# Performance work log

Measured on AMD Instinct MI355X. Metric: run time of the kernel, lower is better.

Reference implementation:

```python
import jax, jax.numpy as jnp
import numpy as np

N_NODES = 100000
N_EDGES = 800000


def gcn_conv(x, W, b, src, dst, ew, n):
    # PyG GCNConv with edge weights and self-loops already included in (src, dst, ew):
    # deg[i] = sum of incoming edge weights at i; norm_e = d^-1/2[src] * w_e * d^-1/2[dst]
    h = x @ W                                                  # [N, F_out]
    deg = jax.ops.segment_sum(ew, dst, num_segments=n)         # [N]
    dinv = jnp.where(deg > 0, jax.lax.rsqrt(deg), 0.0)
    norm = dinv[src] * ew * dinv[dst]                          # [E]
    out = jax.ops.segment_sum(h[src] * norm[:, None], dst, num_segments=n)
    return out + b


def add_self_loops(edge_index, edge_weight, n):
    loop = jnp.arange(n, dtype=edge_index.dtype)
    src = jnp.concatenate([edge_index[0], loop])
    dst = jnp.concatenate([edge_index[1], loop])
    ew = jnp.concatenate([edge_weight, jnp.ones((n,), edge_weight.dtype)])
    return src, dst, ew


def setup_inputs() -> dict:
    key = jax.random.key(0)
    ks = jax.random.split(key, 10)
    x = jax.random.normal(ks[0], (N_NODES, 5), jnp.float32)
    edge_index = jax.random.randint(ks[1], (2, N_EDGES), 0, N_NODES, dtype=jnp.int64)
    edge_weight = jax.random.uniform(ks[2], (N_EDGES,), jnp.float32)
    def glorot(k, fan_in, fan_out):
        s = float(np.sqrt(6.0 / (fan_in + fan_out)))
        return jax.random.uniform(k, (fan_in, fan_out), jnp.float32, -s, s)
    return {
        "x": x,
        "edge_index": edge_index,
        "edge_weight": edge_weight,
        "W1": glorot(ks[3], 5, 320),
        "b1": jnp.zeros((320,), jnp.float32),
        "W2": glorot(ks[4], 320, 160),
        "b2": jnp.zeros((160,), jnp.float32),
        "We": glorot(ks[5], 160, 80),
        "be": jnp.zeros((80,), jnp.float32),
    }


def reference(x, edge_index, edge_weight, W1, b1, W2, b2, We, be):
    n = x.shape[0]
    src, dst, ew = add_self_loops(edge_index, edge_weight, n)
    h = gcn_conv(x, W1, b1, src, dst, ew, n)        # conv1
    h = jax.nn.relu(h)
    h = gcn_conv(h, W2, b2, src, dst, ew, n)        # conv2
    return h @ We + be                              # embed linear
```

## Files before the change

### kernel.cpp

```cpp
#include <hip/hip_runtime.h>

#define NF0 5
#define F1 320
#define F2 160
#define F3 80

typedef float f32x4 __attribute__((ext_vector_type(4)));
typedef _Float16 f16x8 __attribute__((ext_vector_type(8)));


__global__ void k_binA(const void* ei, const float* __restrict__ ew, const int* __restrict__ flag,
                       int* __restrict__ bin_cnt , int2* __restrict__ bins,
                       int bin_stride, int* __restrict__ ovf_n, int* __restrict__ ovf,
                       int ovf_cap, int E) {
    int e = blockIdx.x * blockDim.x + threadIdx.x;
    if (e >= E) return;
    int s, d;
    if (*flag) {
        const long long* p = (const long long*)ei;
        s = (int)p[e]; d = (int)p[E + e];
    } else {
        const int* p = (const int*)ei;
        s = p[e]; d = p[E + e];
    }
    float w = ew[e];
    int b = d >> 8;
    int pos = atomicAdd(&bin_cnt[b * 16], 1);
    if (pos < bin_stride) {
        int2 pk;
        pk.x = s | ((d & 255) << 24);
        pk.y = __float_as_int(w);
        bins[(size_t)b * bin_stride + pos] = pk;
    } else {
        int o = atomicAdd(ovf_n, 1);
        if (o < ovf_cap) {
            ovf[3 * o] = s; ovf[3 * o + 1] = d; ovf[3 * o + 2] = __float_as_int(w);
        }
    }
}

__global__ void k_fixdeg(const int* __restrict__ ovf_n, const int* __restrict__ ovf, int ovf_cap,
                         float* __restrict__ deg) {
    int n = *ovf_n; if (n > ovf_cap) n = ovf_cap;
    for (int j = blockIdx.x * blockDim.x + threadIdx.x; j < n; j += gridDim.x * blockDim.x)
        atomicAdd(&deg[ovf[3 * j + 1]], __int_as_float(ovf[3 * j + 2]));
}


__global__ __launch_bounds__(256) void k_binB1(const int2* __restrict__ bins, int bin_stride,
                                               const int* __restrict__ bin_cnt,
                                               float* __restrict__ deg ,
                                               int N) {
    __shared__ float deg_l[256];
    int b = blockIdx.x, t = threadIdx.x;
    deg_l[t] = 0.f;
    __syncthreads();
    int ne = bin_cnt[b * 16]; if (ne > bin_stride) ne = bin_stride;
    const int2* bp = bins + (size_t)b * bin_stride;
    for (int j = t; j < ne; j += 256) {
        int2 pk = bp[j];
        atomicAdd(&deg_l[((unsigned int)pk.x) >> 24], __int_as_float(pk.y));
    }
    __syncthreads();
    int node = b * 256 + t;
    if (node < N) deg[node] = rsqrtf(deg[node] + 1.0f + deg_l[t]);
}


__global__ __launch_bounds__(256) void k_binB2(const int2* __restrict__ bins, int bin_stride,
                                               const int* __restrict__ bin_cnt,
                                               const float* __restrict__ dinv,
                                               const float* __restrict__ xp,
                                               int* __restrict__ cnt, int2* __restrict__ bucket,
                                               int cap, float* __restrict__ agg1,
                                               int* __restrict__ ovf_n, int* __restrict__ ovf,
                                               int ovf_cap, int N) {
    __shared__ int cnt_l[256];
    __shared__ float dinv_l[256];
    __shared__ float acc_l[256 * NF0];
    int b = blockIdx.x, t = threadIdx.x;
    cnt_l[t] = 0;
    int node0 = b * 256 + t;
    dinv_l[t] = (node0 < N) ? dinv[node0] : 0.f;
    for (int q = t; q < 256 * NF0; q += 256) acc_l[q] = 0.f;
    __syncthreads();

    int ne = bin_cnt[b * 16]; if (ne > bin_stride) ne = bin_stride;
    const int2* bp = bins + (size_t)b * bin_stride;
    for (int j = t; j < ne; j += 256) {
        int2 pk = bp[j];
        int s = pk.x & 0xFFFFFF;
        int dl = ((unsigned int)pk.x) >> 24;
        float w = dinv[s] * __int_as_float(pk.y) * dinv_l[dl];
        int node = b * 256 + dl;
        int pos = atomicAdd(&cnt_l[dl], 1);
        if (pos < cap) {
            int2 out_pk; out_pk.x = s; out_pk.y = __float_as_int(w);
            bucket[(size_t)node * cap + pos] = out_pk;
        } else {
            int o = atomicAdd(ovf_n, 1);
            if (o < ovf_cap) { ovf[3 * o] = s; ovf[3 * o + 1] = node; ovf[3 * o + 2] = pk.y; }
        }
        float4 sv = *(const float4*)(xp + (size_t)s * 8);
        float s4 = xp[(size_t)s * 8 + 4];
        atomicAdd(&acc_l[dl * NF0 + 0], sv.x * w);
        atomicAdd(&acc_l[dl * NF0 + 1], sv.y * w);
        atomicAdd(&acc_l[dl * NF0 + 2], sv.z * w);
        atomicAdd(&acc_l[dl * NF0 + 3], sv.w * w);
        atomicAdd(&acc_l[dl * NF0 + 4], s4 * w);
    }
    __syncthreads();

    if (node0 < N) {
        float di = dinv_l[t];
        float sc = di * di;
        float4 xv = *(const float4*)(xp + (size_t)node0 * 8);
        float x4 = xp[(size_t)node0 * 8 + 4];
        float* op = agg1 + (size_t)node0 * NF0;
        op[0] = acc_l[t * NF0 + 0] + xv.x * sc;
        op[1] = acc_l[t * NF0 + 1] + xv.y * sc;
        op[2] = acc_l[t * NF0 + 2] + xv.z * sc;
        op[3] = acc_l[t * NF0 + 3] + xv.w * sc;
        op[4] = acc_l[t * NF0 + 4] + x4 * sc;
        int c = cnt_l[t]; if (c > cap) c = cap;
        cnt[node0] = c;
    }
}


__global__ void k_prep(const float* __restrict__ x, float* __restrict__ xp, int N, int padxB,
                       const float* __restrict__ W2, const float* __restrict__ We,
                       _Float16* __restrict__ Bh,
                       const float* __restrict__ b2, const float* __restrict__ be,
                       float* __restrict__ bc,
                       const unsigned int* __restrict__ ei32, int E, int* __restrict__ flag) {
    __shared__ int ok;
    int b = blockIdx.x;
    if (b < padxB) {
        int t = b * 256 + threadIdx.x;
        if (t < N * 8) {
            int f = t & 7, i = t >> 3;
            xp[t] = (f < NF0) ? x[i * NF0 + f] : 0.f;
        }
    } else if (b < padxB + 13) {
        int t = (b - padxB) * 256 + threadIdx.x;
        if (t >= 50 * 64) return;
        int fid = t >> 6, lane = t & 63;
        int kk = fid / 5, ct = fid % 5;
        int col = ct * 16 + (lane & 15);
        int row0 = kk * 32 + (lane >> 4) * 8;
        float acc[8] = {0.f, 0.f, 0.f, 0.f, 0.f, 0.f, 0.f, 0.f};
        for (int m = 0; m < F2; ++m) {
            float wv = We[m * F3 + col];
            #pragma unroll
            for (int i = 0; i < 8; ++i)
                acc[i] += W2[(size_t)(row0 + i) * F2 + m] * wv;
        }
        size_t ob = (size_t)t * 8;
        #pragma unroll
        for (int i = 0; i < 8; ++i)
            Bh[ob + i] = (_Float16)acc[i];
    } else if (b == padxB + 13) {
        int j = threadIdx.x;
        if (j < F3) {
            float s = be[j];
            for (int k = 0; k < F2; ++k) s += b2[k] * We[k * F3 + j];
            bc[j] = s;
        }
    } else {
        if (threadIdx.x == 0) ok = 1;
        __syncthreads();
        int npairs = E < 2048 ? E : 2048;
        for (int i = threadIdx.x; i < npairs; i += blockDim.x)
            if (ei32[2 * i + 1] != 0u) ok = 0;
        __syncthreads();
        if (threadIdx.x == 0) *flag = ok;
    }
}

__global__ void k_fixA(const float* __restrict__ x, const float* __restrict__ dinv,
                       const int* __restrict__ ovf_n, int* __restrict__ ovf, int ovf_cap,
                       float* __restrict__ agg1) {
    int n = *ovf_n; if (n > ovf_cap) n = ovf_cap;
    for (int j = blockIdx.x * blockDim.x + threadIdx.x; j < n; j += gridDim.x * blockDim.x) {
        int s = ovf[3 * j], d = ovf[3 * j + 1];
        float w = dinv[s] * __int_as_float(ovf[3 * j + 2]) * dinv[d];
        ovf[3 * j + 2] = __float_as_int(w);
        #pragma unroll
        for (int f = 0; f < NF0; ++f)
            atomicAdd(&agg1[(size_t)d * NF0 + f], x[(size_t)s * NF0 + f] * w);
    }
}


__global__ __launch_bounds__(256) void k_node(const float* __restrict__ agg1,
                                              const float* __restrict__ W1,
                                              const float* __restrict__ b1,
                                              const _Float16* __restrict__ Bh,
                                              _Float16* __restrict__ g, int N) {
    __shared__ float W_l[6 * F1];
    int tid = threadIdx.x;
    for (int i = tid; i < 480; i += 256) {
        float4 v = (i < 400) ? ((const float4*)W1)[i] : ((const float4*)b1)[i - 400];
        ((float4*)W_l)[i] = v;
    }
    __syncthreads();

    int w = tid >> 6, l = tid & 63;
    int nl = l & 15, kg = l >> 4;
    int base = blockIdx.x * 64 + w * 16;
    int n0 = base + nl;

    float a0v[5] = {0.f, 0.f, 0.f, 0.f, 0.f};
    if (n0 < N) {
        const float* ap = agg1 + (size_t)n0 * NF0;
        #pragma unroll
        for (int j = 0; j < 5; ++j) a0v[j] = ap[j];
    }

    f32x4 zero = {0.f, 0.f, 0.f, 0.f};
    f32x4 acc[5] = {zero, zero, zero, zero, zero};
    const f16x8* bhp = (const f16x8*)Bh;

    #pragma unroll
    for (int kk = 0; kk < 10; ++kk) {
        int k0 = kk * 32 + kg * 8;
        float v0[8];
        const float* bb = W_l + 5 * F1 + k0;
        #pragma unroll
        for (int i = 0; i < 8; ++i) v0[i] = bb[i];
        #pragma unroll
        for (int j = 0; j < 5; ++j) {
            const float* wp = W_l + j * F1 + k0;
            float aj0 = a0v[j];
            #pragma unroll
            for (int i = 0; i < 8; ++i) v0[i] += aj0 * wp[i];
        }
        f16x8 ah0, al0;
        #pragma unroll
        for (int i = 0; i < 8; ++i) {
            float t0 = fmaxf(v0[i], 0.f);
            _Float16 h0 = (_Float16)t0;
            ah0[i] = h0;
            al0[i] = (_Float16)(t0 - (float)h0);
        }
        #pragma unroll
        for (int ct = 0; ct < 5; ++ct) {
            f16x8 bf = bhp[(kk * 5 + ct) * 64 + l];
            acc[ct] = __builtin_amdgcn_mfma_f32_16x16x32_f16(ah0, bf, acc[ct], 0, 0, 0);
            acc[ct] = __builtin_amdgcn_mfma_f32_16x16x32_f16(al0, bf, acc[ct], 0, 0, 0);
        }
    }

    #pragma unroll
    for (int ct = 0; ct < 5; ++ct) {
        #pragma unroll
        for (int r = 0; r < 4; ++r) {
            int r0 = base + kg * 4 + r;
            if (r0 < N) g[(size_t)r0 * F3 + ct * 16 + nl] = (_Float16)acc[ct][r];
        }
    }
}


__global__ __launch_bounds__(256) void k_aggB(const _Float16* __restrict__ g,
                                              const float* __restrict__ dinv,
                                              const float* __restrict__ bc,
                                              const int* __restrict__ cnt,
                                              const int2* __restrict__ bucket, int cap,
                                              float* __restrict__ out, int N) {
    int t = blockIdx.x * blockDim.x + threadIdx.x;
    if (t >= 5 * N) return;
    int i = t / 5;
    int c = (t - i * 5) << 4;
    float di = dinv[i];
    float sc = di * di;
    float acc[16];
    {
        const f16x8* sp = (const f16x8*)(g + (size_t)i * F3 + c);
        f16x8 u0 = sp[0], u1 = sp[1];
        const float4* bp = (const float4*)(bc + c);
        float4 q0 = bp[0], q1 = bp[1], q2 = bp[2], q3 = bp[3];
        acc[0]  = (float)u0[0] * sc + q0.x;  acc[1]  = (float)u0[1] * sc + q0.y;
        acc[2]  = (float)u0[2] * sc + q0.z;  acc[3]  = (float)u0[3] * sc + q0.w;
        acc[4]  = (float)u0[4] * sc + q1.x;  acc[5]  = (float)u0[5] * sc + q1.y;
        acc[6]  = (float)u0[6] * sc + q1.z;  acc[7]  = (float)u0[7] * sc + q1.w;
        acc[8]  = (float)u1[0] * sc + q2.x;  acc[9]  = (float)u1[1] * sc + q2.y;
        acc[10] = (float)u1[2] * sc + q2.z;  acc[11] = (float)u1[3] * sc + q2.w;
        acc[12] = (float)u1[4] * sc + q3.x;  acc[13] = (float)u1[5] * sc + q3.y;
        acc[14] = (float)u1[6] * sc + q3.z;  acc[15] = (float)u1[7] * sc + q3.w;
    }
    int cn = cnt[i];
    const int2* row = bucket + (size_t)i * cap;
    #pragma unroll 2
    for (int j = 0; j < cn; ++j) {
        int2 pk = row[j];
        float w = __int_as_float(pk.y);
        const f16x8* sp = (const f16x8*)(g + (size_t)pk.x * F3 + c);
        f16x8 a = sp[0], b8 = sp[1];
        #pragma unroll
        for (int e = 0; e < 8; ++e) {
            acc[e]     += (float)a[e]  * w;
            acc[8 + e] += (float)b8[e] * w;
        }
    }
    float4* op = (float4*)(out + (size_t)i * F3 + c);
    #pragma unroll
    for (int q = 0; q < 4; ++q) {
        float4 v;
        v.x = acc[q * 4 + 0]; v.y = acc[q * 4 + 1]; v.z = acc[q * 4 + 2]; v.w = acc[q * 4 + 3];
        op[q] = v;
    }
}

__global__ void k_fixB(const _Float16* __restrict__ g, const float* __restrict__ dinv,
                       const int* __restrict__ ovf_n, const int* __restrict__ ovf, int ovf_cap,
                       float* __restrict__ out) {
    int n = *ovf_n; if (n > ovf_cap) n = ovf_cap;
    for (int j = blockIdx.x * blockDim.x + threadIdx.x; j < n; j += gridDim.x * blockDim.x) {
        int s = ovf[3 * j], d = ovf[3 * j + 1];
        float w = __int_as_float(ovf[3 * j + 2]);
        for (int f = 0; f < F3; ++f)
            atomicAdd(&out[(size_t)d * F3 + f], (float)g[(size_t)s * F3 + f] * w);
    }
}


static inline size_t align256(size_t x) { return (x + 255) & ~(size_t)255; }

extern "C" void kernel_launch(void* const* d_in, const int* in_sizes, int n_in,
                              void* d_out, int out_size, void* d_ws, size_t ws_size,
                              hipStream_t stream) {
    const float* x  = (const float*)d_in[0];
    const void*  ei = d_in[1];
    const float* ew = (const float*)d_in[2];
    const float* W1 = (const float*)d_in[3];
    const float* b1 = (const float*)d_in[4];
    const float* W2 = (const float*)d_in[5];
    const float* b2 = (const float*)d_in[6];
    const float* We = (const float*)d_in[7];
    const float* be = (const float*)d_in[8];
    float* out = (float*)d_out;

    int N = in_sizes[0] / NF0;
    int E = in_sizes[2];

    const int OVF_CAP = 131072;
    const int BIN_STRIDE = 4096;
    int n_bins = (N + 255) >> 8;

    char* p = (char*)d_ws;
    auto alloc = [&](size_t bytes) { char* r = p; p += align256(bytes); return r; };
    int*   flag  = (int*)alloc(4);
    size_t zints = (size_t)N + 16 + (size_t)n_bins * 16;
    int*   zreg  = (int*)alloc(zints * 4);
    float* deg   = (float*)zreg;
    int*   ovf_n = zreg + N;
    int*   bin_cnt = zreg + N + 16;
    int*   cnt   = (int*)  alloc((size_t)N * 4);
    int*   ovf   = (int*)  alloc((size_t)OVF_CAP * 12);
    int2*  bins  = (int2*) alloc((size_t)n_bins * BIN_STRIDE * 8);
    float* xp    = (float*)alloc((size_t)N * 8 * 4);
    float* agg1  = (float*)alloc((size_t)N * NF0 * 4);
    float* bc    = (float*)alloc((size_t)F3 * 4);
    _Float16* Bh = (_Float16*)alloc((size_t)50 * 64 * 8 * 2);
    _Float16* g  = (_Float16*)alloc((size_t)N * F3 * 2);

    size_t used = (size_t)(p - (char*)d_ws);
    int cap = 24;
    if (ws_size > used) {
        size_t avail = (ws_size - used) / ((size_t)N * 8);
        if (avail < (size_t)cap) cap = (int)avail;
    } else cap = 4;
    if (cap < 4) cap = 4;
    int2* bucket = (int2*)alloc((size_t)N * cap * 8);

    int eb  = (E + 255) / 256;
    int padxB = (N * 8 + 255) / 256;

    hipMemsetAsync(zreg, 0, zints * 4, stream);
    k_prep<<<padxB + 15, 256, 0, stream>>>(x, xp, N, padxB, W2, We, Bh, b2, be, bc,
                                           (const unsigned int*)ei, E, flag);

    k_binA<<<eb, 256, 0, stream>>>(ei, ew, flag, bin_cnt, bins, BIN_STRIDE, ovf_n, ovf, OVF_CAP, E);
    k_fixdeg<<<16, 256, 0, stream>>>(ovf_n, ovf, OVF_CAP, deg);
    k_binB1<<<n_bins, 256, 0, stream>>>(bins, BIN_STRIDE, bin_cnt, deg, N);
    k_binB2<<<n_bins, 256, 0, stream>>>(bins, BIN_STRIDE, bin_cnt, deg, xp, cnt, bucket, cap,
                                        agg1, ovf_n, ovf, OVF_CAP, N);
    k_fixA<<<16, 256, 0, stream>>>(x, deg, ovf_n, ovf, OVF_CAP, agg1);

    k_node<<<(N + 63) / 64, 256, 0, stream>>>(agg1, W1, b1, Bh, g, N);
    k_aggB<<<(5 * N + 255) / 256, 256, 0, stream>>>(g, deg, bc, cnt, bucket, cap, out, N);
    k_fixB<<<16, 256, 0, stream>>>(g, deg, ovf_n, ovf, OVF_CAP, out);
}
```

Baseline: 189.3 us.

## Factor symmetric normalization into node scaling and split edge bins into sub-bins

The symmetric normalization is factored so that source features are pre-scaled by dinv (xp in binB1, g in k_node) and the destination dinv is applied once per node. Edge weights therefore no longer need per-edge dinv gathers. Edge bins are split into 8 sub-bins chosen by block index, to spread the atomic counter contention in binA. The memset and the separate fixdeg and fixA kernels are folded into prep, binB1 and binB2, which now scan the overflow list per block. This cuts launches and global atomics, but every bin block rescans the whole overflow list, and the smaller per-sub-bin capacity may send more edges to overflow.

```diff
diff --git a/kernel.cpp b/kernel.cpp
--- a/kernel.cpp
+++ b/kernel.cpp
@@ -4,131 +4,15 @@
 #define F1 320
 #define F2 160
 #define F3 80
+#define NSUB 8
+#define SUBCAP 512
 
 typedef float f32x4 __attribute__((ext_vector_type(4)));
 typedef _Float16 f16x8 __attribute__((ext_vector_type(8)));
 
 
-__global__ void k_binA(const void* ei, const float* __restrict__ ew, const int* __restrict__ flag,
-                       int* __restrict__ bin_cnt , int2* __restrict__ bins,
-                       int bin_stride, int* __restrict__ ovf_n, int* __restrict__ ovf,
-                       int ovf_cap, int E) {
-    int e = blockIdx.x * blockDim.x + threadIdx.x;
-    if (e >= E) return;
-    int s, d;
-    if (*flag) {
-        const long long* p = (const long long*)ei;
-        s = (int)p[e]; d = (int)p[E + e];
-    } else {
-        const int* p = (const int*)ei;
-        s = p[e]; d = p[E + e];
-    }
-    float w = ew[e];
-    int b = d >> 8;
-    int pos = atomicAdd(&bin_cnt[b * 16], 1);
-    if (pos < bin_stride) {
-        int2 pk;
-        pk.x = s | ((d & 255) << 24);
-        pk.y = __float_as_int(w);
-        bins[(size_t)b * bin_stride + pos] = pk;
-    } else {
-        int o = atomicAdd(ovf_n, 1);
-        if (o < ovf_cap) {
-            ovf[3 * o] = s; ovf[3 * o + 1] = d; ovf[3 * o + 2] = __float_as_int(w);
-        }
-    }
-}
-
-__global__ void k_fixdeg(const int* __restrict__ ovf_n, const int* __restrict__ ovf, int ovf_cap,
-                         float* __restrict__ deg) {
-    int n = *ovf_n; if (n > ovf_cap) n = ovf_cap;
-    for (int j = blockIdx.x * blockDim.x + threadIdx.x; j < n; j += gridDim.x * blockDim.x)
-        atomicAdd(&deg[ovf[3 * j + 1]], __int_as_float(ovf[3 * j + 2]));
-}
-
-
-__global__ __launch_bounds__(256) void k_binB1(const int2* __restrict__ bins, int bin_stride,
-                                               const int* __restrict__ bin_cnt,
-                                               float* __restrict__ deg ,
-                                               int N) {
-    __shared__ float deg_l[256];
-    int b = blockIdx.x, t = threadIdx.x;
-    deg_l[t] = 0.f;
-    __syncthreads();
-    int ne = bin_cnt[b * 16]; if (ne > bin_stride) ne = bin_stride;
-    const int2* bp = bins + (size_t)b * bin_stride;
-    for (int j = t; j < ne; j += 256) {
-        int2 pk = bp[j];
-        atomicAdd(&deg_l[((unsigned int)pk.x) >> 24], __int_as_float(pk.y));
-    }
-    __syncthreads();
-    int node = b * 256 + t;
-    if (node < N) deg[node] = rsqrtf(deg[node] + 1.0f + deg_l[t]);
-}
-
-
-__global__ __launch_bounds__(256) void k_binB2(const int2* __restrict__ bins, int bin_stride,
-                                               const int* __restrict__ bin_cnt,
-                                               const float* __restrict__ dinv,
-                                               const float* __restrict__ xp,
-                                               int* __restrict__ cnt, int2* __restrict__ bucket,
-                                               int cap, float* __restrict__ agg1,
-                                               int* __restrict__ ovf_n, int* __restrict__ ovf,
-                                               int ovf_cap, int N) {
-    __shared__ int cnt_l[256];
-    __shared__ float dinv_l[256];
-    __shared__ float acc_l[256 * NF0];
-    int b = blockIdx.x, t = threadIdx.x;
-    cnt_l[t] = 0;
-    int node0 = b * 256 + t;
-    dinv_l[t] = (node0 < N) ? dinv[node0] : 0.f;
-    for (int q = t; q < 256 * NF0; q += 256) acc_l[q] = 0.f;
-    __syncthreads();
-
-    int ne = bin_cnt[b * 16]; if (ne > bin_stride) ne = bin_stride;
-    const int2* bp = bins + (size_t)b * bin_stride;
-    for (int j = t; j < ne; j += 256) {
-        int2 pk = bp[j];
-        int s = pk.x & 0xFFFFFF;
-        int dl = ((unsigned int)pk.x) >> 24;
-        float w = dinv[s] * __int_as_float(pk.y) * dinv_l[dl];
-        int node = b * 256 + dl;
-        int pos = atomicAdd(&cnt_l[dl], 1);
-        if (pos < cap) {
-            int2 out_pk; out_pk.x = s; out_pk.y = __float_as_int(w);
-            bucket[(size_t)node * cap + pos] = out_pk;
-        } else {
-            int o = atomicAdd(ovf_n, 1);
-            if (o < ovf_cap) { ovf[3 * o] = s; ovf[3 * o + 1] = node; ovf[3 * o + 2] = pk.y; }
-        }
-        float4 sv = *(const float4*)(xp + (size_t)s * 8);
-        float s4 = xp[(size_t)s * 8 + 4];
-        atomicAdd(&acc_l[dl * NF0 + 0], sv.x * w);
-        atomicAdd(&acc_l[dl * NF0 + 1], sv.y * w);
-        atomicAdd(&acc_l[dl * NF0 + 2], sv.z * w);
-        atomicAdd(&acc_l[dl * NF0 + 3], sv.w * w);
-        atomicAdd(&acc_l[dl * NF0 + 4], s4 * w);
-    }
-    __syncthreads();
-
-    if (node0 < N) {
-        float di = dinv_l[t];
-        float sc = di * di;
-        float4 xv = *(const float4*)(xp + (size_t)node0 * 8);
-        float x4 = xp[(size_t)node0 * 8 + 4];
-        float* op = agg1 + (size_t)node0 * NF0;
-        op[0] = acc_l[t * NF0 + 0] + xv.x * sc;
-        op[1] = acc_l[t * NF0 + 1] + xv.y * sc;
-        op[2] = acc_l[t * NF0 + 2] + xv.z * sc;
-        op[3] = acc_l[t * NF0 + 3] + xv.w * sc;
-        op[4] = acc_l[t * NF0 + 4] + x4 * sc;
-        int c = cnt_l[t]; if (c > cap) c = cap;
-        cnt[node0] = c;
-    }
-}
-
-
-__global__ void k_prep(const float* __restrict__ x, float* __restrict__ xp, int N, int padxB,
+__global__ void k_prep(const float* __restrict__ x, float* __restrict__ xp, int N,
+                       int padz, int* __restrict__ zreg, int zwords, int padxB,
                        const float* __restrict__ W2, const float* __restrict__ We,
                        _Float16* __restrict__ Bh,
                        const float* __restrict__ b2, const float* __restrict__ be,
@@ -136,6 +20,12 @@
                        const unsigned int* __restrict__ ei32, int E, int* __restrict__ flag) {
     __shared__ int ok;
     int b = blockIdx.x;
+    if (b < padz) {
+        int t = b * 256 + threadIdx.x;
+        if (t < zwords) zreg[t] = 0;
+        return;
+    }
+    b -= padz;
     if (b < padxB) {
         int t = b * 256 + threadIdx.x;
         if (t < N * 8) {
@@ -178,17 +68,151 @@
     }
 }
 
-__global__ void k_fixA(const float* __restrict__ x, const float* __restrict__ dinv,
-                       const int* __restrict__ ovf_n, int* __restrict__ ovf, int ovf_cap,
-                       float* __restrict__ agg1) {
+
+__global__ void k_binA(const void* ei, const float* __restrict__ ew, const int* __restrict__ flag,
+                       int* __restrict__ bin_cnt , int2* __restrict__ bins,
+                       int n_bins, int* __restrict__ ovf_n, int* __restrict__ ovf,
+                       int ovf_cap, int E) {
+    int e = blockIdx.x * blockDim.x + threadIdx.x;
+    if (e >= E) return;
+    int sub = blockIdx.x & (NSUB - 1);
+    int s, d;
+    if (*flag) {
+        const long long* p = (const long long*)ei;
+        s = (int)p[e]; d = (int)p[E + e];
+    } else {
+        const int* p = (const int*)ei;
+        s = p[e]; d = p[E + e];
+    }
+    float w = ew[e];
+    int b = d >> 8;
+    int pos = atomicAdd(&bin_cnt[(sub * n_bins + b) * 4], 1);
+    if (pos < SUBCAP) {
+        int2 pk;
+        pk.x = s | ((d & 255) << 24);
+        pk.y = __float_as_int(w);
+        bins[(size_t)b * (NSUB * SUBCAP) + sub * SUBCAP + pos] = pk;
+    } else {
+        int o = atomicAdd(ovf_n, 1);
+        if (o < ovf_cap) {
+            ovf[3 * o] = s; ovf[3 * o + 1] = d; ovf[3 * o + 2] = __float_as_int(w);
+        }
+    }
+}
+
+
+__global__ __launch_bounds__(256) void k_binB1(const int2* __restrict__ bins,
+                                               const int* __restrict__ bin_cnt, int n_bins,
+                                               float* __restrict__ dinv, float* __restrict__ xp,
+                                               const int* __restrict__ ovf_n,
+                                               const int* __restrict__ ovf, int ovf_cap, int N) {
+    __shared__ float deg_l[256];
+    int b = blockIdx.x, t = threadIdx.x;
+    deg_l[t] = 0.f;
+    __syncthreads();
+    for (int sub = 0; sub < NSUB; ++sub) {
+        int ne = bin_cnt[(sub * n_bins + b) * 4]; if (ne > SUBCAP) ne = SUBCAP;
+        const int2* bp = bins + (size_t)b * (NSUB * SUBCAP) + sub * SUBCAP;
+        for (int j = t; j < ne; j += 256) {
+            int2 pk = bp[j];
+            atomicAdd(&deg_l[((unsigned int)pk.x) >> 24], __int_as_float(pk.y));
+        }
+    }
     int n = *ovf_n; if (n > ovf_cap) n = ovf_cap;
-    for (int j = blockIdx.x * blockDim.x + threadIdx.x; j < n; j += gridDim.x * blockDim.x) {
-        int s = ovf[3 * j], d = ovf[3 * j + 1];
-        float w = dinv[s] * __int_as_float(ovf[3 * j + 2]) * dinv[d];
-        ovf[3 * j + 2] = __float_as_int(w);
-        #pragma unroll
-        for (int f = 0; f < NF0; ++f)
-            atomicAdd(&agg1[(size_t)d * NF0 + f], x[(size_t)s * NF0 + f] * w);
+    int lo = b * 256;
+    for (int j = t; j < n; j += 256) {
+        int d = ovf[3 * j + 1];
+        if (d >= lo && d < lo + 256)
+            atomicAdd(&deg_l[d - lo], __int_as_float(ovf[3 * j + 2]));
+    }
+    __syncthreads();
+    int node = lo + t;
+    if (node < N) {
+        float di = rsqrtf(1.0f + deg_l[t]);
+        dinv[node] = di;
+        float4* xr = (float4*)(xp + (size_t)node * 8);
+        float4 v0 = xr[0], v1 = xr[1];
+        v0.x *= di; v0.y *= di; v0.z *= di; v0.w *= di;
+        v1.x *= di; v1.y *= di; v1.z *= di; v1.w *= di;
+        xr[0] = v0; xr[1] = v1;
+    }
+}
+
+
+__global__ __launch_bounds__(256) void k_binB2(const int2* __restrict__ bins,
+                                               const int* __restrict__ bin_cnt, int n_bins,
+                                               const float* __restrict__ dinv,
+                                               const float* __restrict__ xp,
+                                               int* __restrict__ cnt, int2* __restrict__ bucket,
+                                               int cap, float* __restrict__ agg1,
+                                               int* __restrict__ ovf_n, int* __restrict__ ovf,
+                                               int ovf_cap, int N) {
+    __shared__ int cnt_l[256];
+    __shared__ float acc_l[256 * NF0];
+    int b = blockIdx.x, t = threadIdx.x;
+    cnt_l[t] = 0;
+    for (int q = t; q < 256 * NF0; q += 256) acc_l[q] = 0.f;
+    int nsnap = *ovf_n; if (nsnap > ovf_cap) nsnap = ovf_cap;
+    __syncthreads();
+    int lo = b * 256;
+
+    for (int j = t; j < nsnap; j += 256) {
+        int d = ovf[3 * j + 1];
+        if (d >= lo && d < lo + 256) {
+            int s = ovf[3 * j];
+            float w = __int_as_float(ovf[3 * j + 2]);
+            float4 sv = *(const float4*)(xp + (size_t)s * 8);
+            float s4 = xp[(size_t)s * 8 + 4];
+            int dl = d - lo;
+            atomicAdd(&acc_l[dl * NF0 + 0], sv.x * w);
+            atomicAdd(&acc_l[dl * NF0 + 1], sv.y * w);
+            atomicAdd(&acc_l[dl * NF0 + 2], sv.z * w);
+            atomicAdd(&acc_l[dl * NF0 + 3], sv.w * w);
+            atomicAdd(&acc_l[dl * NF0 + 4], s4 * w);
+        }
+    }
+
+    for (int sub = 0; sub < NSUB; ++sub) {
+        int ne = bin_cnt[(sub * n_bins + b) * 4]; if (ne > SUBCAP) ne = SUBCAP;
+        const int2* bp = bins + (size_t)b * (NSUB * SUBCAP) + sub * SUBCAP;
+        for (int j = t; j < ne; j += 256) {
+            int2 pk = bp[j];
+            int s = pk.x & 0xFFFFFF;
+            int dl = ((unsigned int)pk.x) >> 24;
+            float w = __int_as_float(pk.y);
+            int node = lo + dl;
+            int pos = atomicAdd(&cnt_l[dl], 1);
+            if (pos < cap) {
+                int2 out_pk; out_pk.x = s; out_pk.y = pk.y;
+                bucket[(size_t)node * cap + pos] = out_pk;
+            } else {
+                int o = atomicAdd(ovf_n, 1);
+                if (o < ovf_cap) { ovf[3 * o] = s; ovf[3 * o + 1] = node; ovf[3 * o + 2] = pk.y; }
+            }
+            float4 sv = *(const float4*)(xp + (size_t)s * 8);
+            float s4 = xp[(size_t)s * 8 + 4];
+            atomicAdd(&acc_l[dl * NF0 + 0], sv.x * w);
+            atomicAdd(&acc_l[dl * NF0 + 1], sv.y * w);
+            atomicAdd(&acc_l[dl * NF0 + 2], sv.z * w);
+            atomicAdd(&acc_l[dl * NF0 + 3], sv.w * w);
+            atomicAdd(&acc_l[dl * NF0 + 4], s4 * w);
+        }
+    }
+    __syncthreads();
+
+    int node = lo + t;
+    if (node < N) {
+        float di = dinv[node];
+        float4 xv = *(const float4*)(xp + (size_t)node * 8);
+        float x4 = xp[(size_t)node * 8 + 4];
+        float* op = agg1 + (size_t)node * NF0;
+        op[0] = di * (acc_l[t * NF0 + 0] + xv.x);
+        op[1] = di * (acc_l[t * NF0 + 1] + xv.y);
+        op[2] = di * (acc_l[t * NF0 + 2] + xv.z);
+        op[3] = di * (acc_l[t * NF0 + 3] + xv.w);
+        op[4] = di * (acc_l[t * NF0 + 4] + x4);
+        int c = cnt_l[t]; if (c > cap) c = cap;
+        cnt[node] = c;
     }
 }
 
@@ -197,6 +221,7 @@
                                               const float* __restrict__ W1,
                                               const float* __restrict__ b1,
                                               const _Float16* __restrict__ Bh,
+                                              const float* __restrict__ dinv,
                                               _Float16* __restrict__ g, int N) {
     __shared__ float W_l[6 * F1];
     int tid = threadIdx.x;
@@ -253,11 +278,13 @@
     }
 
     #pragma unroll
-    for (int ct = 0; ct < 5; ++ct) {
-        #pragma unroll
-        for (int r = 0; r < 4; ++r) {
-            int r0 = base + kg * 4 + r;
-            if (r0 < N) g[(size_t)r0 * F3 + ct * 16 + nl] = (_Float16)acc[ct][r];
+    for (int r = 0; r < 4; ++r) {
+        int r0 = base + kg * 4 + r;
+        if (r0 < N) {
+            float dv = dinv[r0];
+            #pragma unroll
+            for (int ct = 0; ct < 5; ++ct)
+                g[(size_t)r0 * F3 + ct * 16 + nl] = (_Float16)(acc[ct][r] * dv);
         }
     }
 }
@@ -273,23 +300,9 @@
     if (t >= 5 * N) return;
     int i = t / 5;
     int c = (t - i * 5) << 4;
-    float di = dinv[i];
-    float sc = di * di;
     float acc[16];
-    {
-        const f16x8* sp = (const f16x8*)(g + (size_t)i * F3 + c);
-        f16x8 u0 = sp[0], u1 = sp[1];
-        const float4* bp = (const float4*)(bc + c);
-        float4 q0 = bp[0], q1 = bp[1], q2 = bp[2], q3 = bp[3];
-        acc[0]  = (float)u0[0] * sc + q0.x;  acc[1]  = (float)u0[1] * sc + q0.y;
-        acc[2]  = (float)u0[2] * sc + q0.z;  acc[3]  = (float)u0[3] * sc + q0.w;
-        acc[4]  = (float)u0[4] * sc + q1.x;  acc[5]  = (float)u0[5] * sc + q1.y;
-        acc[6]  = (float)u0[6] * sc + q1.z;  acc[7]  = (float)u0[7] * sc + q1.w;
-        acc[8]  = (float)u1[0] * sc + q2.x;  acc[9]  = (float)u1[1] * sc + q2.y;
-        acc[10] = (float)u1[2] * sc + q2.z;  acc[11] = (float)u1[3] * sc + q2.w;
-        acc[12] = (float)u1[4] * sc + q3.x;  acc[13] = (float)u1[5] * sc + q3.y;
-        acc[14] = (float)u1[6] * sc + q3.z;  acc[15] = (float)u1[7] * sc + q3.w;
-    }
+    #pragma unroll
+    for (int e = 0; e < 16; ++e) acc[e] = 0.f;
     int cn = cnt[i];
     const int2* row = bucket + (size_t)i * cap;
     #pragma unroll 2
@@ -304,13 +317,30 @@
             acc[8 + e] += (float)b8[e] * w;
         }
     }
+    float di = dinv[i];
+    const f16x8* sp = (const f16x8*)(g + (size_t)i * F3 + c);
+    f16x8 u0 = sp[0], u1 = sp[1];
+    const float4* bp = (const float4*)(bc + c);
+    float4 q0 = bp[0], q1 = bp[1], q2 = bp[2], q3 = bp[3];
+    float4 o0, o1, o2, o3;
+    o0.x = di * (acc[0]  + (float)u0[0]) + q0.x;
+    o0.y = di * (acc[1]  + (float)u0[1]) + q0.y;
+    o0.z = di * (acc[2]  + (float)u0[2]) + q0.z;
+    o0.w = di * (acc[3]  + (float)u0[3]) + q0.w;
+    o1.x = di * (acc[4]  + (float)u0[4]) + q1.x;
+    o1.y = di * (acc[5]  + (float)u0[5]) + q1.y;
+    o1.z = di * (acc[6]  + (float)u0[6]) + q1.z;
+    o1.w = di * (acc[7]  + (float)u0[7]) + q1.w;
+    o2.x = di * (acc[8]  + (float)u1[0]) + q2.x;
+    o2.y = di * (acc[9]  + (float)u1[1]) + q2.y;
+    o2.z = di * (acc[10] + (float)u1[2]) + q2.z;
+    o2.w = di * (acc[11] + (float)u1[3]) + q2.w;
+    o3.x = di * (acc[12] + (float)u1[4]) + q3.x;
+    o3.y = di * (acc[13] + (float)u1[5]) + q3.y;
+    o3.z = di * (acc[14] + (float)u1[6]) + q3.z;
+    o3.w = di * (acc[15] + (float)u1[7]) + q3.w;
     float4* op = (float4*)(out + (size_t)i * F3 + c);
-    #pragma unroll
-    for (int q = 0; q < 4; ++q) {
-        float4 v;
-        v.x = acc[q * 4 + 0]; v.y = acc[q * 4 + 1]; v.z = acc[q * 4 + 2]; v.w = acc[q * 4 + 3];
-        op[q] = v;
-    }
+    op[0] = o0; op[1] = o1; op[2] = o2; op[3] = o3;
 }
 
 __global__ void k_fixB(const _Float16* __restrict__ g, const float* __restrict__ dinv,
@@ -319,7 +349,7 @@
     int n = *ovf_n; if (n > ovf_cap) n = ovf_cap;
     for (int j = blockIdx.x * blockDim.x + threadIdx.x; j < n; j += gridDim.x * blockDim.x) {
         int s = ovf[3 * j], d = ovf[3 * j + 1];
-        float w = __int_as_float(ovf[3 * j + 2]);
+        float w = dinv[d] * __int_as_float(ovf[3 * j + 2]);
         for (int f = 0; f < F3; ++f)
             atomicAdd(&out[(size_t)d * F3 + f], (float)g[(size_t)s * F3 + f] * w);
     }
@@ -346,20 +376,19 @@
     int E = in_sizes[2];
 
     const int OVF_CAP = 131072;
-    const int BIN_STRIDE = 4096;
     int n_bins = (N + 255) >> 8;
 
     char* p = (char*)d_ws;
     auto alloc = [&](size_t bytes) { char* r = p; p += align256(bytes); return r; };
     int*   flag  = (int*)alloc(4);
-    size_t zints = (size_t)N + 16 + (size_t)n_bins * 16;
-    int*   zreg  = (int*)alloc(zints * 4);
-    float* deg   = (float*)zreg;
-    int*   ovf_n = zreg + N;
-    int*   bin_cnt = zreg + N + 16;
+    int zwords = 16 + NSUB * n_bins * 4;
+    int*   zreg  = (int*)alloc((size_t)zwords * 4);
+    int*   ovf_n = zreg;
+    int*   bin_cnt = zreg + 16;
+    float* dinv  = (float*)alloc((size_t)N * 4);
     int*   cnt   = (int*)  alloc((size_t)N * 4);
     int*   ovf   = (int*)  alloc((size_t)OVF_CAP * 12);
-    int2*  bins  = (int2*) alloc((size_t)n_bins * BIN_STRIDE * 8);
+    int2*  bins  = (int2*) alloc((size_t)n_bins * NSUB * SUBCAP * 8);
     float* xp    = (float*)alloc((size_t)N * 8 * 4);
     float* agg1  = (float*)alloc((size_t)N * NF0 * 4);
     float* bc    = (float*)alloc((size_t)F3 * 4);
@@ -375,21 +404,20 @@
     if (cap < 4) cap = 4;
     int2* bucket = (int2*)alloc((size_t)N * cap * 8);
 
-    int eb  = (E + 255) / 256;
+    int eb    = (E + 255) / 256;
+    int padz  = (zwords + 255) / 256;
     int padxB = (N * 8 + 255) / 256;
 
-    hipMemsetAsync(zreg, 0, zints * 4, stream);
-    k_prep<<<padxB + 15, 256, 0, stream>>>(x, xp, N, padxB, W2, We, Bh, b2, be, bc,
-                                           (const unsigned int*)ei, E, flag);
-
-    k_binA<<<eb, 256, 0, stream>>>(ei, ew, flag, bin_cnt, bins, BIN_STRIDE, ovf_n, ovf, OVF_CAP, E);
-    k_fixdeg<<<16, 256, 0, stream>>>(ovf_n, ovf, OVF_CAP, deg);
-    k_binB1<<<n_bins, 256, 0, stream>>>(bins, BIN_STRIDE, bin_cnt, deg, N);
-    k_binB2<<<n_bins, 256, 0, stream>>>(bins, BIN_STRIDE, bin_cnt, deg, xp, cnt, bucket, cap,
+    k_prep<<<padz + padxB + 15, 256, 0, stream>>>(x, xp, N, padz, zreg, zwords, padxB,
+                                                  W2, We, Bh, b2, be, bc,
+                                                  (const unsigned int*)ei, E, flag);
+
+    k_binA<<<eb, 256, 0, stream>>>(ei, ew, flag, bin_cnt, bins, n_bins, ovf_n, ovf, OVF_CAP, E);
+    k_binB1<<<n_bins, 256, 0, stream>>>(bins, bin_cnt, n_bins, dinv, xp, ovf_n, ovf, OVF_CAP, N);
+    k_binB2<<<n_bins, 256, 0, stream>>>(bins, bin_cnt, n_bins, dinv, xp, cnt, bucket, cap,
                                         agg1, ovf_n, ovf, OVF_CAP, N);
-    k_fixA<<<16, 256, 0, stream>>>(x, deg, ovf_n, ovf, OVF_CAP, agg1);
-
-    k_node<<<(N + 63) / 64, 256, 0, stream>>>(agg1, W1, b1, Bh, g, N);
-    k_aggB<<<(5 * N + 255) / 256, 256, 0, stream>>>(g, deg, bc, cnt, bucket, cap, out, N);
-    k_fixB<<<16, 256, 0, stream>>>(g, deg, ovf_n, ovf, OVF_CAP, out);
-}
+
+    k_node<<<(N + 63) / 64, 256, 0, stream>>>(agg1, W1, b1, Bh, dinv, g, N);
+    k_aggB<<<(5 * N + 255) / 256, 256, 0, stream>>>(g, dinv, bc, cnt, bucket, cap, out, N);
+    k_fixB<<<16, 256, 0, stream>>>(g, dinv, ovf_n, ovf, OVF_CAP, out);
+}
```

New measurement: 182.5 us. 3.6% less time.
